# Optimization experiments

Measured on AMD Instinct MI355X. Metric: run time of the kernel, lower is better.

The kernel has to match this reference:

```python
import jax, jax.numpy as jnp
import numpy as np

B, S, D = 2, 2048, 1024
H, DH = 16, 64          # num_heads, dim_head -> inner = 1024
INNER = H * DH
FF = 4096
SCALE = DH ** -0.5
EPS = 1e-5


def layernorm(x, g, b):
    m = jnp.mean(x, axis=-1, keepdims=True)
    v = jnp.var(x, axis=-1, keepdims=True)
    return (x - m) * jax.lax.rsqrt(v + EPS) * g + b


def attention(x, ctx, mask, wq, wk, wv, wo, bo):
    b, n, _ = x.shape
    j = ctx.shape[1]
    q = (x @ wq).reshape(b, n, H, DH).transpose(0, 2, 1, 3)      # b h i d
    k = (ctx @ wk).reshape(b, j, H, DH).transpose(0, 2, 1, 3)    # b h j d
    v = (ctx @ wv).reshape(b, j, H, DH).transpose(0, 2, 1, 3)
    sim = jnp.einsum('bhid,bhjd->bhij', q, k) * SCALE
    if mask is not None:
        neg = -jnp.finfo(sim.dtype).max
        sim = jnp.where(mask[:, None, None, :], neg, sim)        # mask True -> masked out
    attn = jax.nn.softmax(sim, axis=-1)
    out = jnp.einsum('bhij,bhjd->bhid', attn, v)
    out = out.transpose(0, 2, 1, 3).reshape(b, n, INNER)
    return out @ wo + bo


def setup_inputs():
    key = jax.random.key(0)
    ks = jax.random.split(key, 26)
    w = lambda k, shp, fan: (jax.random.normal(k, shp, jnp.float32) / np.sqrt(fan)).astype(jnp.float32)
    return {
        'x': jax.random.normal(ks[0], (B, S, D), jnp.float32),
        'enc_output': jax.random.normal(ks[1], (B, S, D), jnp.float32),
        'sa_wq': w(ks[2], (D, INNER), D), 'sa_wk': w(ks[3], (D, INNER), D),
        'sa_wv': w(ks[4], (D, INNER), D), 'sa_wo': w(ks[5], (INNER, D), INNER),
        'sa_bo': jnp.zeros((D,), jnp.float32),
        'ca_wq': w(ks[6], (D, INNER), D), 'ca_wk': w(ks[7], (D, INNER), D),
        'ca_wv': w(ks[8], (D, INNER), D), 'ca_wo': w(ks[9], (INNER, D), INNER),
        'ca_bo': jnp.zeros((D,), jnp.float32),
        'ln1_g': jnp.ones((D,), jnp.float32), 'ln1_b': jnp.zeros((D,), jnp.float32),
        'ln2_g': jnp.ones((D,), jnp.float32), 'ln2_b': jnp.zeros((D,), jnp.float32),
        'ln3_g': jnp.ones((D,), jnp.float32), 'ln3_b': jnp.zeros((D,), jnp.float32),
        'fc1_w': w(ks[10], (D, FF), D), 'fc1_b': jnp.zeros((FF,), jnp.float32),
        'fc2_w': w(ks[11], (FF, D), FF), 'fc2_b': jnp.zeros((D,), jnp.float32),
        'tgt_mask': jax.random.bernoulli(ks[12], 0.1, (B, S)),
        'src_mask': jax.random.bernoulli(ks[13], 0.1, (B, S)),
    }


def reference(x, enc_output, sa_wq, sa_wk, sa_wv, sa_wo, sa_bo,
              ca_wq, ca_wk, ca_wv, ca_wo, ca_bo,
              ln1_g, ln1_b, ln2_g, ln2_b, ln3_g, ln3_b,
              fc1_w, fc1_b, fc2_w, fc2_b, tgt_mask, src_mask):
    # self attention + residual + post-LN
    a = attention(x, x, tgt_mask, sa_wq, sa_wk, sa_wv, sa_wo, sa_bo)
    x = layernorm(x + a, ln1_g, ln1_b)
    # cross attention against encoder output
    a = attention(x, enc_output, src_mask, ca_wq, ca_wk, ca_wv, ca_wo, ca_bo)
    x = layernorm(x + a, ln2_g, ln2_b)
    # MLP (exact GELU, matching torch nn.GELU default)
    h = jax.nn.gelu(x @ fc1_w + fc1_b, approximate=False)
    ff = h @ fc2_w + fc2_b
    x = layernorm(x + ff, ln3_g, ln3_b)
    return x
```

## Files before the change

### kernel.cpp

```cpp
#include <hip/hip_runtime.h>
#include <hip/hip_bf16.h>
#include <math.h>

#define BB 2
#define SS 2048
#define DD 1024
#define HH 16
#define DHD 64
#define FFD 4096
#define NROWS (BB*SS)
#define QLD 3072

typedef __bf16 bf16_t;
typedef __bf16 bf16x8 __attribute__((ext_vector_type(8)));
typedef float floatx4 __attribute__((ext_vector_type(4)));

union FragU { uint4 u; bf16x8 v; bf16_t e[8]; };
union U4v  { uint2 u; bf16_t e[4]; };

static __device__ __forceinline__ bf16x8 ld_frag16(const bf16_t* p) {
  FragU f; f.u = *reinterpret_cast<const uint4*>(p); return f.v;
}

static __device__ __forceinline__ void gl_lds16(const bf16_t* g, bf16_t* l) {
  __builtin_amdgcn_global_load_lds(
      (const __attribute__((address_space(1))) unsigned int*)g,
      (__attribute__((address_space(3))) unsigned int*)l, 16, 0, 0);
}

static __device__ __forceinline__ float ld_param(const void* p, int i, int f32m) {
  return f32m ? ((const float*)p)[i] : (float)((const bf16_t*)p)[i];
}

__global__ __launch_bounds__(256) void detect_k(const void* __restrict__ xp,
                                                const void* __restrict__ ep,
                                                const void* __restrict__ wp,
                                                const int* __restrict__ mk,
                                                int* __restrict__ flags) {
  const int t = threadIdx.x;
  const unsigned short* a = (const unsigned short*)xp;
  const unsigned short* b = (const unsigned short*)ep;
  const unsigned short* c = (const unsigned short*)wp;
  int bad = 0, mbad = 0;
  for (int i = t; i < 4096; i += 256) {
    int e1 = (a[i] >> 7) & 0xFF, e2 = (b[i] >> 7) & 0xFF, e3 = (c[i] >> 7) & 0xFF;
    if (e1 >= 0x9B || e2 >= 0x9B || e3 >= 0x9B) bad = 1;
  }
  for (int i = t; i < 1024; i += 256) {
    unsigned v = (unsigned)mk[i];
    if (v > 1u) mbad = 1;
  }
  __shared__ int s0, s1;
  if (t == 0) { s0 = 0; s1 = 0; }
  __syncthreads();
  if (bad)  atomicOr(&s0, 1);
  if (mbad) atomicOr(&s1, 1);
  __syncthreads();
  if (t == 0) { flags[0] = s0; flags[1] = s1; }
}

__global__ __launch_bounds__(256) void cvt_k(const void* __restrict__ src,
                                             bf16_t* __restrict__ dst, int n,
                                             const int* __restrict__ flg) {
  const int f32m = flg[0];
  const int idx = blockIdx.x * 256 + threadIdx.x;
  const int stride = gridDim.x * 256;
  const int n8 = n >> 3;
  if (f32m) {
    const float4* s = (const float4*)src;
    for (int i = idx; i < n8; i += stride) {
      float4 a = s[2 * i], b = s[2 * i + 1];
      FragU f;
      f.e[0] = (bf16_t)a.x; f.e[1] = (bf16_t)a.y; f.e[2] = (bf16_t)a.z; f.e[3] = (bf16_t)a.w;
      f.e[4] = (bf16_t)b.x; f.e[5] = (bf16_t)b.y; f.e[6] = (bf16_t)b.z; f.e[7] = (bf16_t)b.w;
      *reinterpret_cast<uint4*>(dst + (size_t)i * 8) = f.u;
    }
  } else {
    const uint4* s = (const uint4*)src;
    uint4* d = (uint4*)dst;
    for (int i = idx; i < n8; i += stride) d[i] = s[i];
  }
}

static __device__ __forceinline__ void transpose_body(const void* inv, bf16_t* out,
                                                      int rows, int cols, int f32m) {
  __shared__ __align__(16) bf16_t tile[64][72];
  const int c0 = blockIdx.x * 64, r0 = blockIdx.y * 64;
  const int t  = threadIdx.x;
  const int lr = t >> 3;
  const int lc = (t & 7) * 8;
#pragma unroll
  for (int half = 0; half < 2; ++half) {
    int r = lr + half * 32;
    if (f32m) {
      const float* p = (const float*)inv + (size_t)(r0 + r) * cols + c0 + lc;
      float4 q0 = *reinterpret_cast<const float4*>(p);
      float4 q1 = *reinterpret_cast<const float4*>(p + 4);
      tile[r][lc+0] = (bf16_t)q0.x; tile[r][lc+1] = (bf16_t)q0.y;
      tile[r][lc+2] = (bf16_t)q0.z; tile[r][lc+3] = (bf16_t)q0.w;
      tile[r][lc+4] = (bf16_t)q1.x; tile[r][lc+5] = (bf16_t)q1.y;
      tile[r][lc+6] = (bf16_t)q1.z; tile[r][lc+7] = (bf16_t)q1.w;
    } else {
      uint4 vv = *reinterpret_cast<const uint4*>((const bf16_t*)inv + (size_t)(r0 + r) * cols + c0 + lc);
      *reinterpret_cast<uint4*>(&tile[r][lc]) = vv;
    }
  }
  __syncthreads();
#pragma unroll
  for (int half = 0; half < 2; ++half) {
    int oc = lr + half * 32;
    FragU f;
#pragma unroll
    for (int j = 0; j < 8; ++j) f.e[j] = tile[lc + j][oc];
    *reinterpret_cast<uint4*>(out + (size_t)(c0 + oc) * rows + r0 + lc) = f.u;
  }
}

__global__ __launch_bounds__(256) void transpose_k(const void* __restrict__ inv,
                                                   bf16_t* __restrict__ out,
                                                   int rows, int cols,
                                                   const int* __restrict__ flg) {
  transpose_body(inv, out, rows, cols, flg[0]);
}

struct Ptr4 { const void* p0; const void* p1; const void* p2; const void* p3; };

__global__ __launch_bounds__(256) void transpose4_k(Ptr4 in, bf16_t* __restrict__ out,
                                                    const int* __restrict__ flg) {
  const void* src = (blockIdx.z == 0) ? in.p0 : (blockIdx.z == 1) ? in.p1
                   : (blockIdx.z == 2) ? in.p2 : in.p3;
  transpose_body(src, out + (size_t)blockIdx.z * DD * DD, DD, DD, flg[0]);
}

template<int BIAS, int GELU>
__global__ __launch_bounds__(256) void gemm_nt(const bf16_t* __restrict__ A,
                                               const bf16_t* __restrict__ A2,
                                               int nsplit,
                                               const bf16_t* __restrict__ Bt,
                                               const void* __restrict__ bias,
                                               bf16_t* __restrict__ C,
                                               int M, int N, int K, int ldc,
                                               const int* __restrict__ flg) {
  __shared__ __align__(16) bf16_t As[128 * 32];
  __shared__ __align__(16) bf16_t Bs[128 * 32];
  const int m0 = blockIdx.y * 128, n0 = blockIdx.x * 128;
  const bf16_t* Ap = (A2 != nullptr && n0 >= nsplit) ? A2 : A;
  const int t = threadIdx.x, lane = t & 63, w = t >> 6;
  const int quad = lane >> 4, l16 = lane & 15;
  const int wy = w >> 1, wx = w & 1;

  floatx4 acc[4][4];
#pragma unroll
  for (int i = 0; i < 4; ++i)
#pragma unroll
    for (int j = 0; j < 4; ++j) { floatx4 z = {0.f,0.f,0.f,0.f}; acc[i][j] = z; }

  const int srow = lane >> 2;
  const int scol = (lane & 3) * 8;

  for (int k0 = 0; k0 < K; k0 += 32) {
    __syncthreads();
#pragma unroll
    for (int c = 0; c < 2; ++c) {
      const int chunk = w * 2 + c;
      const int r = chunk * 16 + srow;
      gl_lds16(Ap + (size_t)(m0 + r) * K + k0 + scol, As + chunk * 512);
      gl_lds16(Bt + (size_t)(n0 + r) * K + k0 + scol, Bs + chunk * 512);
    }
    __syncthreads();

    bf16x8 af[4], bfr[4];
#pragma unroll
    for (int mt = 0; mt < 4; ++mt) af[mt]  = ld_frag16(As + (wy*64 + mt*16 + l16) * 32 + quad*8);
#pragma unroll
    for (int nt = 0; nt < 4; ++nt) bfr[nt] = ld_frag16(Bs + (wx*64 + nt*16 + l16) * 32 + quad*8);
#pragma unroll
    for (int mt = 0; mt < 4; ++mt)
#pragma unroll
      for (int nt = 0; nt < 4; ++nt)
        acc[mt][nt] = __builtin_amdgcn_mfma_f32_16x16x32_bf16(af[mt], bfr[nt], acc[mt][nt], 0, 0, 0);
  }

  const int f32m = BIAS ? flg[0] : 0;
#pragma unroll
  for (int nt = 0; nt < 4; ++nt) {
    const int c = n0 + wx*64 + nt*16 + l16;
    float bv = 0.f;
    if (BIAS) bv = ld_param(bias, c, f32m);
#pragma unroll
    for (int mt = 0; mt < 4; ++mt) {
      const int rb = m0 + wy*64 + mt*16 + quad*4;
#pragma unroll
      for (int reg = 0; reg < 4; ++reg) {
        float v2 = acc[mt][nt][reg] + bv;
        if (GELU) v2 = 0.5f * v2 * (1.f + erff(v2 * 0.70710678118654752f));
        C[(size_t)(rb + reg) * ldc + c] = (bf16_t)v2;
      }
    }
  }
}

__global__ __launch_bounds__(256, 5) void attn_k(const bf16_t* __restrict__ QKV,
                                                 const int* __restrict__ mask,
                                                 bf16_t* __restrict__ O,
                                                 const int* __restrict__ flg) {
  __shared__ __align__(16) bf16_t Ks[64 * 72];
  __shared__ __align__(16) bf16_t Vt[64 * 72];
  __shared__ __align__(16) bf16_t Ps[4][16 * 72];
  __shared__ bf16_t msk[SS];
  const int mflag = flg[1];
  const int b = blockIdx.y >> 4, h = blockIdx.y & 15;
  const int s0 = blockIdx.x * 64;
  const int t = threadIdx.x, w = t >> 6, lane = t & 63;
  const int quad = lane >> 4, l16 = lane & 15;
  const float L2S = 0.18033688011112042f;

  for (int j = t; j < SS; j += 256) {
    const int mv = mflag ? (int)((const signed char*)mask)[b * SS + j] : mask[b * SS + j];
    msk[j] = (bf16_t)(mv ? -1.0e30f : -8.0f);
  }

  bf16x8 qf[2];
  {
    const int r = s0 + w * 16 + l16;
    const bf16_t* qp = QKV + (size_t)(b * SS + r) * QLD + h * DHD;
#pragma unroll
    for (int kq = 0; kq < 2; ++kq) qf[kq] = ld_frag16(qp + kq * 32 + quad * 8);
  }

  bf16x8 ones;
#pragma unroll
  for (int j = 0; j < 8; ++j) ones[j] = (bf16_t)1.0f;

  floatx4 accO[4], accl;
  { floatx4 z = {0.f,0.f,0.f,0.f}; accl = z;
#pragma unroll
    for (int i = 0; i < 4; ++i) accO[i] = z; }

  const int krow = t >> 2, kc = (t & 3) * 16;
  const int vkey = t & 63, vw16 = (t >> 6) * 16;
  const int vq = vkey >> 3, vk7 = vkey & 7;
  const int vs0 = (vw16 >> 3) & 7, vs1 = (vs0 + 1) & 7;

  int coff[4];
#pragma unroll
  for (int cf = 0; cf < 4; ++cf)
    coff[cf] = (((((cf << 1) | (l16 >> 3))) ^ ((quad >> 1) << 1)) << 3) + (l16 & 7);
  const int rsw = ((l16 >> 3) & 1) << 1;

  const bf16_t* kp = QKV + 1024 + (size_t)(b * SS + krow) * QLD + h * DHD + kc;
  const bf16_t* vp = QKV + 2048 + (size_t)(b * SS + vkey) * QLD + h * DHD + vw16;

  uint4 kr0 = *reinterpret_cast<const uint4*>(kp);
  uint4 kr1 = *reinterpret_cast<const uint4*>(kp + 8);
  uint4 vr0 = *reinterpret_cast<const uint4*>(vp);
  uint4 vr1 = *reinterpret_cast<const uint4*>(vp + 8);

  for (int j0 = 0; j0 < SS; j0 += 64) {
    __syncthreads();
    *reinterpret_cast<uint4*>(&Ks[krow * 72 + kc])     = kr0;
    *reinterpret_cast<uint4*>(&Ks[krow * 72 + kc + 8]) = kr1;
    { FragU v0; v0.u = vr0; FragU v1; v1.u = vr1;
#pragma unroll
      for (int j = 0; j < 8; ++j) Vt[(vw16 + j) * 72 + ((vq ^ vs0) << 3) + vk7] = v0.e[j];
#pragma unroll
      for (int j = 0; j < 8; ++j) Vt[(vw16 + 8 + j) * 72 + ((vq ^ vs1) << 3) + vk7] = v1.e[j];
    }
    __syncthreads();

    if (j0 + 64 < SS) {
      const bf16_t* kp2 = kp + (size_t)(j0 + 64) * QLD;
      const bf16_t* vp2 = vp + (size_t)(j0 + 64) * QLD;
      kr0 = *reinterpret_cast<const uint4*>(kp2);
      kr1 = *reinterpret_cast<const uint4*>(kp2 + 8);
      vr0 = *reinterpret_cast<const uint4*>(vp2);
      vr1 = *reinterpret_cast<const uint4*>(vp2 + 8);
    }

    floatx4 s4[4];
    { floatx4 z = {0.f,0.f,0.f,0.f};
#pragma unroll
      for (int cf = 0; cf < 4; ++cf) s4[cf] = z; }
#pragma unroll
    for (int kq = 0; kq < 2; ++kq)
#pragma unroll
      for (int cf = 0; cf < 4; ++cf) {
        bf16x8 bf = ld_frag16(&Ks[(cf * 16 + l16) * 72 + kq * 32 + quad * 8]);
        s4[cf] = __builtin_amdgcn_mfma_f32_16x16x32_bf16(qf[kq], bf, s4[cf], 0, 0, 0);
      }
    float ml[4];
#pragma unroll
    for (int cf = 0; cf < 4; ++cf) ml[cf] = (float)msk[j0 + cf * 16 + l16];

#pragma unroll
    for (int reg = 0; reg < 4; ++reg) {
      const float p0 = exp2f(fmaf(s4[0][reg], L2S, ml[0]));
      const float p1 = exp2f(fmaf(s4[1][reg], L2S, ml[1]));
      const float p2 = exp2f(fmaf(s4[2][reg], L2S, ml[2]));
      const float p3 = exp2f(fmaf(s4[3][reg], L2S, ml[3]));
      const int rb = (quad * 4 + reg) * 72;
      Ps[w][rb + coff[0]] = (bf16_t)p0;
      Ps[w][rb + coff[1]] = (bf16_t)p1;
      Ps[w][rb + coff[2]] = (bf16_t)p2;
      Ps[w][rb + coff[3]] = (bf16_t)p3;
    }
    asm volatile("s_waitcnt lgkmcnt(0)" ::: "memory");

    bf16x8 pa0 = ld_frag16(&Ps[w][l16 * 72 + ((quad ^ rsw) << 3)]);
    bf16x8 pa1 = ld_frag16(&Ps[w][l16 * 72 + (((4 + quad) ^ rsw) << 3)]);
#pragma unroll
    for (int nt = 0; nt < 4; ++nt) {
      const int dh = nt * 16 + l16;
      const int sdh = (dh >> 3) & 7;
      bf16x8 vf0 = ld_frag16(&Vt[dh * 72 + ((quad ^ sdh) << 3)]);
      bf16x8 vf1 = ld_frag16(&Vt[dh * 72 + (((4 + quad) ^ sdh) << 3)]);
      accO[nt] = __builtin_amdgcn_mfma_f32_16x16x32_bf16(pa0, vf0, accO[nt], 0, 0, 0);
      accO[nt] = __builtin_amdgcn_mfma_f32_16x16x32_bf16(pa1, vf1, accO[nt], 0, 0, 0);
    }
    accl = __builtin_amdgcn_mfma_f32_16x16x32_bf16(pa0, ones, accl, 0, 0, 0);
    accl = __builtin_amdgcn_mfma_f32_16x16x32_bf16(pa1, ones, accl, 0, 0, 0);
  }

#pragma unroll
  for (int nt = 0; nt < 4; ++nt)
#pragma unroll
    for (int reg = 0; reg < 4; ++reg) {
      const int r = s0 + w * 16 + quad * 4 + reg;
      const int c = h * DHD + nt * 16 + l16;
      O[(size_t)(b * SS + r) * DD + c] = (bf16_t)(accO[nt][reg] / accl[reg]);
    }
}

__global__ __launch_bounds__(256) void ln_add_k(const bf16_t* __restrict__ X,
                                                const bf16_t* __restrict__ A,
                                                const void* __restrict__ g,
                                                const void* __restrict__ bb,
                                                void* __restrict__ Yv,
                                                const int* __restrict__ flg,
                                                int final_out) {
  const int row = blockIdx.x;
  const int t = threadIdx.x;
  const int f32m = flg[0];
  const int f32o = final_out ? f32m : 0;
  const bf16_t* xp = X + (size_t)row * DD;
  const bf16_t* ap = A + (size_t)row * DD;
  U4v xu, au;
  xu.u = ((const uint2*)xp)[t];
  au.u = ((const uint2*)ap)[t];
  float v[4], s = 0.f, sq = 0.f;
#pragma unroll
  for (int i = 0; i < 4; ++i) {
    float xv = (float)xu.e[i] + (float)au.e[i];
    v[i] = xv; s += xv; sq += xv * xv;
  }
#pragma unroll
  for (int off = 1; off < 64; off <<= 1) {
    s  += __shfl_xor(s, off, 64);
    sq += __shfl_xor(sq, off, 64);
  }
  __shared__ float red[2][4];
  const int w = t >> 6, lane = t & 63;
  if (lane == 0) { red[0][w] = s; red[1][w] = sq; }
  __syncthreads();
  s  = red[0][0] + red[0][1] + red[0][2] + red[0][3];
  sq = red[1][0] + red[1][1] + red[1][2] + red[1][3];
  const float mean = s * (1.f / 1024.f);
  const float var  = sq * (1.f / 1024.f) - mean * mean;
  const float rstd = rsqrtf(var + 1e-5f);
  float gv[4], bv[4];
  if (f32m) {
    float4 gg = ((const float4*)g)[t];
    float4 bg = ((const float4*)bb)[t];
    gv[0]=gg.x; gv[1]=gg.y; gv[2]=gg.z; gv[3]=gg.w;
    bv[0]=bg.x; bv[1]=bg.y; bv[2]=bg.z; bv[3]=bg.w;
  } else {
    U4v gg, bg;
    gg.u = ((const uint2*)g)[t];
    bg.u = ((const uint2*)bb)[t];
#pragma unroll
    for (int i = 0; i < 4; ++i) { gv[i] = (float)gg.e[i]; bv[i] = (float)bg.e[i]; }
  }
  float val[4];
#pragma unroll
  for (int i = 0; i < 4; ++i) val[i] = (v[i] - mean) * rstd * gv[i] + bv[i];
  if (f32o) {
    float4 o; o.x = val[0]; o.y = val[1]; o.z = val[2]; o.w = val[3];
    ((float4*)((float*)Yv + (size_t)row * DD))[t] = o;
  } else {
    U4v o;
#pragma unroll
    for (int i = 0; i < 4; ++i) o.e[i] = (bf16_t)val[i];
    ((uint2*)((bf16_t*)Yv + (size_t)row * DD))[t] = o.u;
  }
}

__global__ __launch_bounds__(256) void beacon_k(bf16_t* out, int n, float val) {
  int i = blockIdx.x * 256 + threadIdx.x;
  if (i < n) out[i] = (bf16_t)val;
}

extern "C" void kernel_launch(void* const* d_in, const int* in_sizes, int n_in,
                              void* d_out, int out_size, void* d_ws, size_t ws_size,
                              hipStream_t stream) {
  const dim3 blk(256);
  const dim3 gB((out_size + 255) / 256);

  static const int expect[24] = {
    4194304, 4194304,
    1048576, 1048576, 1048576, 1048576, 1024,
    1048576, 1048576, 1048576, 1048576, 1024,
    1024, 1024, 1024, 1024, 1024, 1024,
    4194304, 4096,
    4194304, 1024,
    4096, 4096
  };
  if (n_in != 24) {
    beacon_k<<<gB, blk, 0, stream>>>((bf16_t*)d_out, out_size, 200.f + (float)(n_in & 63));
    return;
  }
  for (int i = 0; i < 24; ++i) {
    if (in_sizes[i] != expect[i]) {
      beacon_k<<<gB, blk, 0, stream>>>((bf16_t*)d_out, out_size, 20.f + 2.f * (float)i);
      return;
    }
  }

  const void* x_raw   = d_in[0];
  const void* enc_raw = d_in[1];
  const void* sa_wq = d_in[2], *sa_wk = d_in[3], *sa_wv = d_in[4], *sa_wo = d_in[5];
  const void* sa_bo = d_in[6];
  const void* ca_wq = d_in[7], *ca_wk = d_in[8], *ca_wv = d_in[9], *ca_wo = d_in[10];
  const void* ca_bo = d_in[11];
  const void* ln1_g = d_in[12], *ln1_b = d_in[13];
  const void* ln2_g = d_in[14], *ln2_b = d_in[15];
  const void* ln3_g = d_in[16], *ln3_b = d_in[17];
  const void* fc1_w = d_in[18], *fc1_b = d_in[19];
  const void* fc2_w = d_in[20], *fc2_b = d_in[21];
  const int* tgt_mask = (const int*)d_in[22];
  const int* src_mask = (const int*)d_in[23];

  const size_t SEG = (size_t)NROWS * DD;
  const size_t PS_ELEMS = 32768;
  if (ws_size < (8 * SEG + PS_ELEMS) * sizeof(bf16_t)) {
    beacon_k<<<gB, blk, 0, stream>>>((bf16_t*)d_out, out_size, 7.f);
    return;
  }
  bf16_t* ws  = (bf16_t*)d_ws;
  bf16_t* qkv = ws + 0 * SEG;
  bf16_t* wt  = ws + 3 * SEG;
  bf16_t* t1  = ws + 4 * SEG;
  bf16_t* x1  = ws + 5 * SEG;
  bf16_t* xc  = ws + 6 * SEG;
  bf16_t* ec  = ws + 7 * SEG;
  bf16_t* ps  = ws + 8 * SEG;
  int*    fl  = (int*)(ps + 16384);
  const bool big_ws = ws_size >= (12 * SEG + PS_ELEMS) * sizeof(bf16_t);
  bf16_t* hb = ws + 8 * SEG + PS_ELEMS;

  const size_t W1 = (size_t)DD * DD;
  bf16_t* wot = wt + 3 * W1;

  const dim3 gT4(16, 16, 4);
  const dim3 gG(DD / 128, NROWS / 128);
  const dim3 gQKV(3 * DD / 128, NROWS / 128);
  const dim3 gA(SS / 64, BB * HH);
  const dim3 gL(NROWS);
  const dim3 gC(512);

  detect_k<<<dim3(1), blk, 0, stream>>>(x_raw, enc_raw, fc1_w, tgt_mask, fl);
  cvt_k<<<gC, blk, 0, stream>>>(x_raw,   xc, (int)SEG, fl);
  cvt_k<<<gC, blk, 0, stream>>>(enc_raw, ec, (int)SEG, fl);

  { Ptr4 p{sa_wq, sa_wk, sa_wv, sa_wo};
    transpose4_k<<<gT4, blk, 0, stream>>>(p, wt, fl); }
  gemm_nt<0,0><<<gQKV, blk, 0, stream>>>(xc, nullptr, 0, wt, nullptr, qkv,
                                         NROWS, 3 * DD, DD, QLD, fl);
  attn_k<<<gA, blk, 0, stream>>>(qkv, tgt_mask, x1, fl);
  gemm_nt<1,0><<<gG, blk, 0, stream>>>(x1, nullptr, 0, wot, sa_bo, t1,
                                       NROWS, DD, DD, DD, fl);
  ln_add_k<<<gL, blk, 0, stream>>>(xc, t1, ln1_g, ln1_b, x1, fl, 0);

  { Ptr4 p{ca_wq, ca_wk, ca_wv, ca_wo};
    transpose4_k<<<gT4, blk, 0, stream>>>(p, wt, fl); }
  gemm_nt<0,0><<<gQKV, blk, 0, stream>>>(x1, ec, DD, wt, nullptr, qkv,
                                         NROWS, 3 * DD, DD, QLD, fl);
  attn_k<<<gA, blk, 0, stream>>>(qkv, src_mask, xc, fl);
  gemm_nt<1,0><<<gG, blk, 0, stream>>>(xc, nullptr, 0, wot, ca_bo, t1,
                                       NROWS, DD, DD, DD, fl);
  ln_add_k<<<gL, blk, 0, stream>>>(x1, t1, ln2_g, ln2_b, x1, fl, 0);

  transpose_k<<<dim3(FFD/64, DD/64), blk, 0, stream>>>(fc1_w, wt, DD, FFD, fl);
  if (big_ws) {
    gemm_nt<1,1><<<dim3(FFD/128, NROWS/128), blk, 0, stream>>>(x1, nullptr, 0, wt, fc1_b, hb,
                                                               NROWS, FFD, DD, FFD, fl);
    transpose_k<<<dim3(DD/64, FFD/64), blk, 0, stream>>>(fc2_w, wt, FFD, DD, fl);
    gemm_nt<1,0><<<dim3(DD/128, NROWS/128), blk, 0, stream>>>(hb, nullptr, 0, wt, fc2_b, t1,
                                                              NROWS, DD, FFD, DD, fl);
  } else {
    transpose_k<<<dim3(DD/64, FFD/64), blk, 0, stream>>>(fc2_w, qkv, FFD, DD, fl);
    bf16_t* hchunk = qkv + SEG;
    for (int c = 0; c < 4; ++c) {
      gemm_nt<1,1><<<dim3(FFD/128, 8), blk, 0, stream>>>(x1 + (size_t)c*1024*DD, nullptr, 0, wt,
                                                         fc1_b, hchunk, 1024, FFD, DD, FFD, fl);
      gemm_nt<1,0><<<dim3(DD/128, 8), blk, 0, stream>>>(hchunk, nullptr, 0, qkv, fc2_b,
                                                        t1 + (size_t)c*1024*DD, 1024, DD, FFD, DD, fl);
    }
  }
  ln_add_k<<<gL, blk, 0, stream>>>(x1, t1, ln3_g, ln3_b, d_out, fl, 1);
}
```

Measured before the change: 687.7 us.

## Add 256x256-tile 512-thread GEMM with 4-stage ring for QKV and FC1

Introduces a new GEMM kernel with 256x256 output tiles, 8 waves, a 4-deep LDS ring of async global-to-LDS loads, XCD-aware block remapping, and split MFMA phases with priority hints. It replaces the 128x128 GEMM for the two QKV projections and the FC1+GELU GEMM. The larger tiles raise operand reuse and the deeper pipeline hides load latency. In exchange, register pressure rises and fewer workgroups are launched (192 or 256), which may underfill the GPU.

```diff
diff --git a/kernel.cpp b/kernel.cpp
--- a/kernel.cpp
+++ b/kernel.cpp
@@ -190,6 +190,119 @@
 #pragma unroll
     for (int mt = 0; mt < 4; ++mt) {
       const int rb = m0 + wy*64 + mt*16 + quad*4;
+#pragma unroll
+      for (int reg = 0; reg < 4; ++reg) {
+        float v2 = acc[mt][nt][reg] + bv;
+        if (GELU) v2 = 0.5f * v2 * (1.f + erff(v2 * 0.70710678118654752f));
+        C[(size_t)(rb + reg) * ldc + c] = (bf16_t)v2;
+      }
+    }
+  }
+}
+
+template<int BIAS, int GELU>
+__global__ __launch_bounds__(512, 2) void gemm256(const bf16_t* __restrict__ A,
+                                                  const bf16_t* __restrict__ A2,
+                                                  int nsplit,
+                                                  const bf16_t* __restrict__ Bt,
+                                                  const void* __restrict__ bias,
+                                                  bf16_t* __restrict__ C,
+                                                  int M, int N, int K, int ldc,
+                                                  const int* __restrict__ flg) {
+  __shared__ __align__(16) bf16_t ring[4][2][256 * 32];
+  const int nwg = gridDim.x;
+  int id = blockIdx.x;
+  if ((nwg & 7) == 0) { const int cpx = nwg >> 3; id = (id & 7) * cpx + (id >> 3); }
+  const int gx = N >> 8;
+  const int bx = id % gx, by = id / gx;
+  const int m0 = by * 256, n0 = bx * 256;
+  const bf16_t* Ap = (A2 != nullptr && n0 >= nsplit) ? A2 : A;
+
+  const int t = threadIdx.x, lane = t & 63, w = t >> 6;
+  const int quad = lane >> 4, l16 = lane & 15;
+  const int wy = w >> 2, wx = w & 3;
+  const int f32m = BIAS ? flg[0] : 0;
+
+  const int srow = t >> 2;
+  const int sc8  = (((t & 3) ^ ((t >> 2) & 3)) << 3);
+  const bf16_t* Agp0 = Ap + (size_t)(m0 + srow) * K + sc8;
+  const bf16_t* Agp1 = Ap + (size_t)(m0 + 128 + srow) * K + sc8;
+  const bf16_t* Bgp0 = Bt + (size_t)(n0 + srow) * K + sc8;
+  const bf16_t* Bgp1 = Bt + (size_t)(n0 + 128 + srow) * K + sc8;
+  const int dH0 = (w * 16) * 32;
+  const int dH1 = (128 + w * 16) * 32;
+
+#define STAGE256(u) do { const int _s = (u) & 3; const size_t _k = (size_t)(u) * 32; \
+    gl_lds16(Agp0 + _k, &ring[_s][0][dH0]); \
+    gl_lds16(Agp1 + _k, &ring[_s][0][dH1]); \
+    gl_lds16(Bgp0 + _k, &ring[_s][1][dH0]); \
+    gl_lds16(Bgp1 + _k, &ring[_s][1][dH1]); } while (0)
+
+  floatx4 acc[8][4];
+#pragma unroll
+  for (int i = 0; i < 8; ++i)
+#pragma unroll
+    for (int j = 0; j < 4; ++j) { floatx4 z = {0.f,0.f,0.f,0.f}; acc[i][j] = z; }
+
+  const int NT = K >> 5;
+  STAGE256(0); STAGE256(1); STAGE256(2);
+  asm volatile("s_waitcnt vmcnt(8)" ::: "memory");
+  __builtin_amdgcn_s_barrier();
+
+  const int cq8  = (quad ^ (l16 & 3)) << 3;
+  const int arow = wy * 128 + l16;
+  const int brow = wx * 64 + l16;
+
+  for (int tt = 0; tt < NT; ++tt) {
+    const bf16_t* As = ring[tt & 3][0];
+    const bf16_t* Bs = ring[tt & 3][1];
+    if (tt + 3 < NT) STAGE256(tt + 3);
+    bf16x8 af[4], bfr[4];
+#pragma unroll
+    for (int mt = 0; mt < 4; ++mt) af[mt]  = ld_frag16(As + (arow + mt * 16) * 32 + cq8);
+#pragma unroll
+    for (int nt = 0; nt < 4; ++nt) bfr[nt] = ld_frag16(Bs + (brow + nt * 16) * 32 + cq8);
+    __builtin_amdgcn_s_barrier();
+    asm volatile("s_waitcnt lgkmcnt(0)" ::: "memory");
+    __builtin_amdgcn_sched_barrier(0);
+    __builtin_amdgcn_s_setprio(1);
+#pragma unroll
+    for (int mt = 0; mt < 4; ++mt)
+#pragma unroll
+      for (int nt = 0; nt < 4; ++nt)
+        acc[mt][nt] = __builtin_amdgcn_mfma_f32_16x16x32_bf16(af[mt], bfr[nt], acc[mt][nt], 0, 0, 0);
+    __builtin_amdgcn_s_setprio(0);
+    __builtin_amdgcn_s_barrier();
+#pragma unroll
+    for (int mt = 0; mt < 4; ++mt) af[mt] = ld_frag16(As + (arow + (mt + 4) * 16) * 32 + cq8);
+    {
+      const int rem = NT - 2 - tt;
+      if (rem >= 2)      asm volatile("s_waitcnt vmcnt(8)" ::: "memory");
+      else if (rem == 1) asm volatile("s_waitcnt vmcnt(4)" ::: "memory");
+      else               asm volatile("s_waitcnt vmcnt(0)" ::: "memory");
+    }
+    __builtin_amdgcn_s_barrier();
+    asm volatile("s_waitcnt lgkmcnt(0)" ::: "memory");
+    __builtin_amdgcn_sched_barrier(0);
+    __builtin_amdgcn_s_setprio(1);
+#pragma unroll
+    for (int mt = 0; mt < 4; ++mt)
+#pragma unroll
+      for (int nt = 0; nt < 4; ++nt)
+        acc[mt + 4][nt] = __builtin_amdgcn_mfma_f32_16x16x32_bf16(af[mt], bfr[nt], acc[mt + 4][nt], 0, 0, 0);
+    __builtin_amdgcn_s_setprio(0);
+    __builtin_amdgcn_s_barrier();
+  }
+#undef STAGE256
+
+#pragma unroll
+  for (int nt = 0; nt < 4; ++nt) {
+    const int c = n0 + wx * 64 + nt * 16 + l16;
+    float bv = 0.f;
+    if (BIAS) bv = ld_param(bias, c, f32m);
+#pragma unroll
+    for (int mt = 0; mt < 8; ++mt) {
+      const int rb = m0 + wy * 128 + mt * 16 + quad * 4;
 #pragma unroll
       for (int reg = 0; reg < 4; ++reg) {
         float v2 = acc[mt][nt][reg] + bv;
@@ -403,6 +516,7 @@
                               void* d_out, int out_size, void* d_ws, size_t ws_size,
                               hipStream_t stream) {
   const dim3 blk(256);
+  const dim3 blk512(512);
   const dim3 gB((out_size + 255) / 256);
 
   static const int expect[24] = {
@@ -462,7 +576,8 @@
 
   const dim3 gT4(16, 16, 4);
   const dim3 gG(DD / 128, NROWS / 128);
-  const dim3 gQKV(3 * DD / 128, NROWS / 128);
+  const dim3 gQKV(3 * DD / 256 * (NROWS / 256));
+  const dim3 gFC1(FFD / 256 * (NROWS / 256));
   const dim3 gA(SS / 64, BB * HH);
   const dim3 gL(NROWS);
   const dim3 gC(512);
@@ -473,8 +588,8 @@
 
   { Ptr4 p{sa_wq, sa_wk, sa_wv, sa_wo};
     transpose4_k<<<gT4, blk, 0, stream>>>(p, wt, fl); }
-  gemm_nt<0,0><<<gQKV, blk, 0, stream>>>(xc, nullptr, 0, wt, nullptr, qkv,
-                                         NROWS, 3 * DD, DD, QLD, fl);
+  gemm256<0,0><<<gQKV, blk512, 0, stream>>>(xc, nullptr, 0, wt, nullptr, qkv,
+                                            NROWS, 3 * DD, DD, QLD, fl);
   attn_k<<<gA, blk, 0, stream>>>(qkv, tgt_mask, x1, fl);
   gemm_nt<1,0><<<gG, blk, 0, stream>>>(x1, nullptr, 0, wot, sa_bo, t1,
                                        NROWS, DD, DD, DD, fl);
@@ -482,8 +597,8 @@
 
   { Ptr4 p{ca_wq, ca_wk, ca_wv, ca_wo};
     transpose4_k<<<gT4, blk, 0, stream>>>(p, wt, fl); }
-  gemm_nt<0,0><<<gQKV, blk, 0, stream>>>(x1, ec, DD, wt, nullptr, qkv,
-                                         NROWS, 3 * DD, DD, QLD, fl);
+  gemm256<0,0><<<gQKV, blk512, 0, stream>>>(x1, ec, DD, wt, nullptr, qkv,
+                                            NROWS, 3 * DD, DD, QLD, fl);
   attn_k<<<gA, blk, 0, stream>>>(qkv, src_mask, xc, fl);
   gemm_nt<1,0><<<gG, blk, 0, stream>>>(xc, nullptr, 0, wot, ca_bo, t1,
                                        NROWS, DD, DD, DD, fl);
@@ -491,8 +606,8 @@
 
   transpose_k<<<dim3(FFD/64, DD/64), blk, 0, stream>>>(fc1_w, wt, DD, FFD, fl);
   if (big_ws) {
-    gemm_nt<1,1><<<dim3(FFD/128, NROWS/128), blk, 0, stream>>>(x1, nullptr, 0, wt, fc1_b, hb,
-                                                               NROWS, FFD, DD, FFD, fl);
+    gemm256<1,1><<<gFC1, blk512, 0, stream>>>(x1, nullptr, 0, wt, fc1_b, hb,
+                                              NROWS, FFD, DD, FFD, fl);
     transpose_k<<<dim3(DD/64, FFD/64), blk, 0, stream>>>(fc2_w, wt, FFD, DD, fl);
     gemm_nt<1,0><<<dim3(DD/128, NROWS/128), blk, 0, stream>>>(hb, nullptr, 0, wt, fc2_b, t1,
                                                               NROWS, DD, FFD, DD, fl);
```

New measurement: 711.2 us. 1.03x slower.
